# Performance work log

Measured on AMD Instinct MI355X. Metric: run time of the kernel, lower is better.

Reference implementation:

```python
import jax, jax.numpy as jnp
import numpy as np

FEATURE_DIM = 2048
NUM_HEADS = 16
NUM_KV_HEADS = 4
HEAD_DIM = 128
NEG = -1e9  # additive mask value for disallowed positions


def setup_inputs() -> dict:
    key = jax.random.key(0)
    ks = jax.random.split(key, 10)
    B, S = 1, 4096
    q_dim = NUM_HEADS * HEAD_DIM
    kv_dim = NUM_KV_HEADS * HEAD_DIM
    hidden_states = jax.random.normal(ks[0], (B, S, FEATURE_DIM), dtype=jnp.float32)
    # additive causal mask (B, 1, S, S): 0 on/below diagonal, large negative above
    causal = jnp.triu(jnp.full((S, S), NEG, dtype=jnp.float32), k=1)
    attention_mask = jnp.broadcast_to(causal, (B, 1, S, S))
    sd = 0.02
    Wq = jax.random.normal(ks[1], (q_dim, FEATURE_DIM), dtype=jnp.float32) * sd
    bq = jnp.zeros((q_dim,), dtype=jnp.float32)
    Wk = jax.random.normal(ks[2], (kv_dim, FEATURE_DIM), dtype=jnp.float32) * sd
    bk = jnp.zeros((kv_dim,), dtype=jnp.float32)
    Wv = jax.random.normal(ks[3], (kv_dim, FEATURE_DIM), dtype=jnp.float32) * sd
    bv = jnp.zeros((kv_dim,), dtype=jnp.float32)
    Wo = jax.random.normal(ks[4], (FEATURE_DIM, FEATURE_DIM), dtype=jnp.float32) * sd
    bo = jnp.zeros((FEATURE_DIM,), dtype=jnp.float32)
    return {
        "hidden_states": hidden_states,
        "attention_mask": attention_mask,
        "Wq": Wq, "bq": bq, "Wk": Wk, "bk": bk,
        "Wv": Wv, "bv": bv, "Wo": Wo, "bo": bo,
    }


def reference(hidden_states, attention_mask, Wq, bq, Wk, bk, Wv, bv, Wo, bo):
    B, S, _ = hidden_states.shape
    groups = NUM_HEADS // NUM_KV_HEADS
    scale = 1.0 / np.sqrt(HEAD_DIM)
    sigmoid_bias = jnp.asarray(-np.log(float(S)), dtype=hidden_states.dtype)

    # projections -> (B, H, S, D)
    q = (hidden_states @ Wq.T + bq).reshape(B, S, NUM_HEADS, HEAD_DIM).transpose(0, 2, 1, 3)
    k = (hidden_states @ Wk.T + bk).reshape(B, S, NUM_KV_HEADS, HEAD_DIM).transpose(0, 2, 1, 3)
    v = (hidden_states @ Wv.T + bv).reshape(B, S, NUM_KV_HEADS, HEAD_DIM).transpose(0, 2, 1, 3)

    # GQA: repeat kv heads to match query heads
    k = jnp.repeat(k, groups, axis=1)
    v = jnp.repeat(v, groups, axis=1)

    # sigmoid attention: QK^T * scale + mask + (-log S), sigmoid, then @V
    scores = jnp.einsum('bhqd,bhkd->bhqk', q, k) * scale
    scores = scores + attention_mask[:, :, :, :S]
    attn = jax.nn.sigmoid(scores + sigmoid_bias)
    out = jnp.einsum('bhqk,bhkd->bhqd', attn, v)

    out = out.transpose(0, 2, 1, 3).reshape(B, S, NUM_HEADS * HEAD_DIM)
    return out @ Wo.T + bo
```

## Files before the change

kernel.cpp:

```cpp
#include <hip/hip_runtime.h>

typedef __attribute__((ext_vector_type(8))) __bf16 bf16x8;
typedef __attribute__((ext_vector_type(4))) __bf16 bf16x4;
typedef __attribute__((ext_vector_type(4))) float  f32x4;

#define MFMA16(a, b, c) __builtin_amdgcn_mfma_f32_16x16x32_bf16((a), (b), (c), 0, 0, 0)

__device__ __forceinline__ void async16(const void* g, void* lds) {
    __builtin_amdgcn_global_load_lds(
        (__attribute__((address_space(1))) void*)(g),
        (__attribute__((address_space(3))) void*)(lds),
        16, 0, 0);
}

__global__ void cast_f32_bf16(const float* __restrict__ in, __bf16* __restrict__ out, int n) {
    int i = (blockIdx.x * blockDim.x + threadIdx.x) * 4;
    if (i >= n) return;
    f32x4 v = *(const f32x4*)(in + i);
    bf16x4 o;
    o[0] = (__bf16)v[0]; o[1] = (__bf16)v[1]; o[2] = (__bf16)v[2]; o[3] = (__bf16)v[3];
    *(bf16x4*)(out + i) = o;
}

#define BM 128
#define BN 128
#define BKK 32

template <typename OutT>
__global__ __launch_bounds__(256, 2) void gemm_bt(
    const __bf16* __restrict__ A,
    const __bf16* __restrict__ B0, OutT* __restrict__ C0, const float* __restrict__ b0, int N0,
    const __bf16* __restrict__ B1, OutT* __restrict__ C1, const float* __restrict__ b1, int N1,
    const __bf16* __restrict__ B2, OutT* __restrict__ C2, const float* __restrict__ b2, int N2,
    int K, bool transC2)
{
    const __bf16* Bm; OutT* Cm; const float* bias; int N;
    int z = blockIdx.z;
    if (z == 0)      { Bm = B0; Cm = C0; bias = b0; N = N0; }
    else if (z == 1) { Bm = B1; Cm = C1; bias = b1; N = N1; }
    else             { Bm = B2; Cm = C2; bias = b2; N = N2; }

    int n0 = blockIdx.x * BN;
    if (n0 >= N) return;
    int m0 = blockIdx.y * BM;

    __shared__ alignas(16) __bf16 As[BM * BKK];
    __shared__ alignas(16) __bf16 Bs[BN * BKK];

    int tid = threadIdx.x;
    int wv = tid >> 6, ln = tid & 63;
    int lr = ln >> 2, lc = ln & 3;
    int fr = ln & 15, fh = ln >> 4;

    int wr = wv >> 1, wc = wv & 1;

    f32x4 acc[4][4];
#pragma unroll
    for (int i = 0; i < 4; ++i)
#pragma unroll
        for (int j = 0; j < 4; ++j) acc[i][j] = (f32x4){0.f, 0.f, 0.f, 0.f};

    const __bf16* Ag = A  + (size_t)m0 * K;
    const __bf16* Bg = Bm + (size_t)n0 * K;

    for (int k0 = 0; k0 < K; k0 += BKK) {
#pragma unroll
        for (int half = 0; half < 2; ++half) {
            int row = wv * 32 + half * 16 + lr;
            async16(Ag + (size_t)row * K + k0 + lc * 8, &As[(wv * 32 + half * 16) * BKK]);
            async16(Bg + (size_t)row * K + k0 + lc * 8, &Bs[(wv * 32 + half * 16) * BKK]);
        }
        __syncthreads();

        bf16x8 af[4], bfr[4];
#pragma unroll
        for (int i = 0; i < 4; ++i) af[i]  = *(const bf16x8*)&As[(wr * 64 + i * 16 + fr) * BKK + fh * 8];
#pragma unroll
        for (int j = 0; j < 4; ++j) bfr[j] = *(const bf16x8*)&Bs[(wc * 64 + j * 16 + fr) * BKK + fh * 8];
#pragma unroll
        for (int i = 0; i < 4; ++i)
#pragma unroll
            for (int j = 0; j < 4; ++j)
                acc[i][j] = MFMA16(af[i], bfr[j], acc[i][j]);
        __syncthreads();
    }

    if constexpr (sizeof(OutT) == 2) {
        if (transC2 && z == 2) {
            const int M = (int)gridDim.y * BM;
            __bf16* Ct = (__bf16*)Cm;
#pragma unroll
            for (int j = 0; j < 4; ++j) {
                int col = n0 + wc * 64 + j * 16 + fr;
                float bv = bias[col];
#pragma unroll
                for (int i = 0; i < 4; ++i) {
                    int rbase = m0 + wr * 64 + i * 16 + fh * 4;
                    bf16x4 o;
#pragma unroll
                    for (int rq = 0; rq < 4; ++rq) o[rq] = (__bf16)(acc[i][j][rq] + bv);
                    *(bf16x4*)&Ct[(size_t)col * M + rbase] = o;
                }
            }
            return;
        }
    }

#pragma unroll
    for (int j = 0; j < 4; ++j) {
        int col = n0 + wc * 64 + j * 16 + fr;
        float bv = bias[col];
#pragma unroll
        for (int i = 0; i < 4; ++i) {
            int rbase = m0 + wr * 64 + i * 16 + fh * 4;
#pragma unroll
            for (int r = 0; r < 4; ++r) {
                float v = acc[i][j][r] + bv;
                Cm[(size_t)(rbase + r) * N + col] = (OutT)v;
            }
        }
    }
}

__global__ __launch_bounds__(256, 4) void attn_sigmoid(
    const __bf16* __restrict__ Qg, const __bf16* __restrict__ Kg,
    const __bf16* __restrict__ Vtg, __bf16* __restrict__ AO)
{
    const float SCALE = 0.08838834764831845f;
    const float SBIAS = -8.31776616671934f;

    int id = blockIdx.x;
    int rr = id >> 8, u = id & 255;
    int h = u & 15, g = u >> 4;
    int qt = (rr == 0) ? 63 - g : (rr == 1) ? 32 + g : (rr == 2) ? 31 - g : g;
    int kvh = h >> 2;

    int tid = threadIdx.x;
    int wv = tid >> 6, ln = tid & 63;
    int fr = ln & 15, fh = ln >> 4;

    __shared__ alignas(16) char KsB[16384];
    __shared__ alignas(16) char VtB[16384];
    __shared__ alignas(16) char PsB[8192];

    bf16x8 qf[4];
    {
        const __bf16* qp = Qg + (size_t)(qt * 64 + wv * 16 + fr) * 2048 + h * 128 + fh * 8;
#pragma unroll
        for (int dk = 0; dk < 4; ++dk) qf[dk] = *(const bf16x8*)(qp + dk * 32);
    }

    f32x4 oacc[8];
#pragma unroll
    for (int dn = 0; dn < 8; ++dn) oacc[dn] = (f32x4){0.f, 0.f, 0.f, 0.f};

    int nkt = qt + 1;
    for (int kt = 0; kt < nkt; ++kt) {
        {
            char* ksl = KsB + wv * 4096;
            char* vtl = VtB + wv * 4096;
#pragma unroll
            for (int i = 0; i < 4; ++i) {
                int r = wv * 16 + i * 4 + (ln >> 4);
                int c = (ln & 15) ^ (r & 15);
                async16(Kg + (size_t)(kt * 64 + r) * 512 + kvh * 128 + c * 8, ksl + i * 1024);
            }
#pragma unroll
            for (int i = 0; i < 4; ++i) {
                int d = wv * 32 + i * 8 + (ln >> 3);
                int c = (ln & 7) ^ (d & 7);
                async16(Vtg + (size_t)(kvh * 128 + d) * 4096 + kt * 64 + c * 8, vtl + i * 1024);
            }
        }
        __syncthreads();

        bool needmask = (kt == qt);
#pragma unroll
        for (int nj = 0; nj < 4; ++nj) {
            bf16x8 kf[4];
            int key = nj * 16 + fr;
#pragma unroll
            for (int dk = 0; dk < 4; ++dk)
                kf[dk] = *(const bf16x8*)(KsB + key * 256 + (((dk * 4 + fh) ^ (key & 15)) << 4));
            f32x4 sa = (f32x4){0.f, 0.f, 0.f, 0.f};
#pragma unroll
            for (int dk = 0; dk < 4; ++dk) sa = MFMA16(qf[dk], kf[dk], sa);
            int kr = nj * 16 + fr;
#pragma unroll
            for (int r = 0; r < 4; ++r) {
                int ql = wv * 16 + fh * 4 + r;
                float x = sa[r] * SCALE + SBIAS;
                float p = __fdividef(1.f, 1.f + __expf(-x));
                if (needmask && kr > ql) p = 0.f;
                *(__bf16*)(PsB + ql * 128 + (((kr >> 3) ^ (ql & 7)) << 4) + (kr & 7) * 2) = (__bf16)p;
            }
        }

        bf16x8 pf[2];
        {
            int q = wv * 16 + fr;
#pragma unroll
            for (int kk = 0; kk < 2; ++kk)
                pf[kk] = *(const bf16x8*)(PsB + q * 128 + (((kk * 4 + fh) ^ (q & 7)) << 4));
        }
#pragma unroll
        for (int dn = 0; dn < 8; ++dn) {
            int d = dn * 16 + fr;
            bf16x8 vf0 = *(const bf16x8*)(VtB + d * 128 + ((fh ^ (d & 7)) << 4));
            bf16x8 vf1 = *(const bf16x8*)(VtB + d * 128 + (((4 + fh) ^ (d & 7)) << 4));
            oacc[dn] = MFMA16(pf[0], vf0, oacc[dn]);
            oacc[dn] = MFMA16(pf[1], vf1, oacc[dn]);
        }
        __syncthreads();
    }

#pragma unroll
    for (int dn = 0; dn < 8; ++dn)
#pragma unroll
        for (int r = 0; r < 4; ++r)
            AO[(size_t)(qt * 64 + wv * 16 + fh * 4 + r) * 2048 + h * 128 + dn * 16 + fr]
                = (__bf16)oacc[dn][r];
}

extern "C" void kernel_launch(void* const* d_in, const int* in_sizes, int n_in,
                              void* d_out, int out_size, void* d_ws, size_t ws_size,
                              hipStream_t stream)
{
    const float* X  = (const float*)d_in[0];
    const float* Wq = (const float*)d_in[2];
    const float* bq = (const float*)d_in[3];
    const float* Wk = (const float*)d_in[4];
    const float* bk = (const float*)d_in[5];
    const float* Wv = (const float*)d_in[6];
    const float* bv = (const float*)d_in[7];
    const float* Wo = (const float*)d_in[8];
    const float* bo = (const float*)d_in[9];
    float* Out = (float*)d_out;

    if (ws_size < 54525952u) return;

    char* ws = (char*)d_ws;
    __bf16* Xb  = (__bf16*)(ws + 0);
    __bf16* Qb  = (__bf16*)(ws + 16777216);
    __bf16* Kb  = (__bf16*)(ws + 33554432);
    __bf16* Vb  = (__bf16*)(ws + 37748736);
    __bf16* Wqb = (__bf16*)(ws + 41943040);
    __bf16* Wkb = (__bf16*)(ws + 50331648);
    __bf16* Wvb = (__bf16*)(ws + 52428800);
    __bf16* AOb = Xb;
    __bf16* Wob = Wqb;

    cast_f32_bf16<<<8192, 256, 0, stream>>>(X,  Xb,  8388608);
    cast_f32_bf16<<<4096, 256, 0, stream>>>(Wq, Wqb, 4194304);
    cast_f32_bf16<<<1024, 256, 0, stream>>>(Wk, Wkb, 1048576);
    cast_f32_bf16<<<1024, 256, 0, stream>>>(Wv, Wvb, 1048576);

    gemm_bt<__bf16><<<dim3(16, 32, 3), 256, 0, stream>>>(Xb,
        Wqb, Qb, bq, 2048,
        Wkb, Kb, bk, 512,
        Wvb, Vb, bv, 512, 2048, true);

    cast_f32_bf16<<<4096, 256, 0, stream>>>(Wo, Wob, 4194304);

    attn_sigmoid<<<1024, 256, 0, stream>>>(Qb, Kb, Vb, AOb);

    gemm_bt<float><<<dim3(16, 32, 1), 256, 0, stream>>>(AOb,
        Wob, Out, bo, 2048,
        nullptr, nullptr, nullptr, 0,
        nullptr, nullptr, nullptr, 0, 2048, false);
}
```

Baseline: 461.0 us.

## Double query tile per attention block to reuse K/V tiles, use exp2/rcp sigmoid

Each attention block now handles 128 query rows (two 16-row sub-tiles per wave) instead of 64, so every K/V tile loaded into LDS feeds twice the MFMA work. The grid halves to 512 blocks, the causal scheduling order is simplified, and launch bounds drop to 3 blocks per SM to allow for the extra registers. The sigmoid is rewritten as a fused exp2 with folded scale and bias constants plus a hardware reciprocal. The trade-off is lower occupancy and coarser load balance across blocks of different causal length.

```diff
diff --git a/kernel.cpp b/kernel.cpp
--- a/kernel.cpp
+++ b/kernel.cpp
@@ -122,17 +122,17 @@
     }
 }
 
-__global__ __launch_bounds__(256, 4) void attn_sigmoid(
+__global__ __launch_bounds__(256, 3) void attn_sigmoid(
     const __bf16* __restrict__ Qg, const __bf16* __restrict__ Kg,
     const __bf16* __restrict__ Vtg, __bf16* __restrict__ AO)
 {
-    const float SCALE = 0.08838834764831845f;
-    const float SBIAS = -8.31776616671934f;
+    const float C1 = -0.12752551286084110f;
+    const float C2 = 12.0f;
 
     int id = blockIdx.x;
     int rr = id >> 8, u = id & 255;
     int h = u & 15, g = u >> 4;
-    int qt = (rr == 0) ? 63 - g : (rr == 1) ? 32 + g : (rr == 2) ? 31 - g : g;
+    int qt = rr ? g : 31 - g;
     int kvh = h >> 2;
 
     int tid = threadIdx.x;
@@ -141,20 +141,23 @@
 
     __shared__ alignas(16) char KsB[16384];
     __shared__ alignas(16) char VtB[16384];
-    __shared__ alignas(16) char PsB[8192];
-
-    bf16x8 qf[4];
-    {
-        const __bf16* qp = Qg + (size_t)(qt * 64 + wv * 16 + fr) * 2048 + h * 128 + fh * 8;
-#pragma unroll
-        for (int dk = 0; dk < 4; ++dk) qf[dk] = *(const bf16x8*)(qp + dk * 32);
-    }
-
-    f32x4 oacc[8];
-#pragma unroll
-    for (int dn = 0; dn < 8; ++dn) oacc[dn] = (f32x4){0.f, 0.f, 0.f, 0.f};
-
-    int nkt = qt + 1;
+    __shared__ alignas(16) char PsB[16384];
+
+    bf16x8 qf[2][4];
+#pragma unroll
+    for (int mi = 0; mi < 2; ++mi) {
+        const __bf16* qp = Qg + (size_t)(qt * 128 + wv * 32 + mi * 16 + fr) * 2048 + h * 128 + fh * 8;
+#pragma unroll
+        for (int dk = 0; dk < 4; ++dk) qf[mi][dk] = *(const bf16x8*)(qp + dk * 32);
+    }
+
+    f32x4 oacc[2][8];
+#pragma unroll
+    for (int mi = 0; mi < 2; ++mi)
+#pragma unroll
+        for (int dn = 0; dn < 8; ++dn) oacc[mi][dn] = (f32x4){0.f, 0.f, 0.f, 0.f};
+
+    int nkt = 2 * qt + 2;
     for (int kt = 0; kt < nkt; ++kt) {
         {
             char* ksl = KsB + wv * 4096;
@@ -174,7 +177,7 @@
         }
         __syncthreads();
 
-        bool needmask = (kt == qt);
+        bool needmask = (kt >= 2 * qt);
 #pragma unroll
         for (int nj = 0; nj < 4; ++nj) {
             bf16x8 kf[4];
@@ -182,44 +185,55 @@
 #pragma unroll
             for (int dk = 0; dk < 4; ++dk)
                 kf[dk] = *(const bf16x8*)(KsB + key * 256 + (((dk * 4 + fh) ^ (key & 15)) << 4));
-            f32x4 sa = (f32x4){0.f, 0.f, 0.f, 0.f};
-#pragma unroll
-            for (int dk = 0; dk < 4; ++dk) sa = MFMA16(qf[dk], kf[dk], sa);
             int kr = nj * 16 + fr;
-#pragma unroll
-            for (int r = 0; r < 4; ++r) {
-                int ql = wv * 16 + fh * 4 + r;
-                float x = sa[r] * SCALE + SBIAS;
-                float p = __fdividef(1.f, 1.f + __expf(-x));
-                if (needmask && kr > ql) p = 0.f;
-                *(__bf16*)(PsB + ql * 128 + (((kr >> 3) ^ (ql & 7)) << 4) + (kr & 7) * 2) = (__bf16)p;
-            }
-        }
-
-        bf16x8 pf[2];
-        {
-            int q = wv * 16 + fr;
+            int keyg = kt * 64 + kr;
+#pragma unroll
+            for (int mi = 0; mi < 2; ++mi) {
+                f32x4 sa = (f32x4){0.f, 0.f, 0.f, 0.f};
+#pragma unroll
+                for (int dk = 0; dk < 4; ++dk) sa = MFMA16(qf[mi][dk], kf[dk], sa);
+                int qb = wv * 32 + mi * 16 + fh * 4;
+#pragma unroll
+                for (int r = 0; r < 4; ++r) {
+                    int ql = qb + r;
+                    float e = __builtin_amdgcn_exp2f(fmaf(sa[r], C1, C2));
+                    float p = __builtin_amdgcn_rcpf(1.f + e);
+                    if (needmask && keyg > qt * 128 + ql) p = 0.f;
+                    *(__bf16*)(PsB + ql * 128 + (((kr >> 3) ^ (ql & 7)) << 4) + (kr & 7) * 2) = (__bf16)p;
+                }
+            }
+        }
+
+        bf16x8 pf[2][2];
+#pragma unroll
+        for (int mi = 0; mi < 2; ++mi) {
+            int q = wv * 32 + mi * 16 + fr;
 #pragma unroll
             for (int kk = 0; kk < 2; ++kk)
-                pf[kk] = *(const bf16x8*)(PsB + q * 128 + (((kk * 4 + fh) ^ (q & 7)) << 4));
+                pf[mi][kk] = *(const bf16x8*)(PsB + q * 128 + (((kk * 4 + fh) ^ (q & 7)) << 4));
         }
 #pragma unroll
         for (int dn = 0; dn < 8; ++dn) {
             int d = dn * 16 + fr;
             bf16x8 vf0 = *(const bf16x8*)(VtB + d * 128 + ((fh ^ (d & 7)) << 4));
             bf16x8 vf1 = *(const bf16x8*)(VtB + d * 128 + (((4 + fh) ^ (d & 7)) << 4));
-            oacc[dn] = MFMA16(pf[0], vf0, oacc[dn]);
-            oacc[dn] = MFMA16(pf[1], vf1, oacc[dn]);
-        }
-        __syncthreads();
-    }
-
-#pragma unroll
-    for (int dn = 0; dn < 8; ++dn)
-#pragma unroll
-        for (int r = 0; r < 4; ++r)
-            AO[(size_t)(qt * 64 + wv * 16 + fh * 4 + r) * 2048 + h * 128 + dn * 16 + fr]
-                = (__bf16)oacc[dn][r];
+#pragma unroll
+            for (int mi = 0; mi < 2; ++mi) {
+                oacc[mi][dn] = MFMA16(pf[mi][0], vf0, oacc[mi][dn]);
+                oacc[mi][dn] = MFMA16(pf[mi][1], vf1, oacc[mi][dn]);
+            }
+        }
+        __syncthreads();
+    }
+
+#pragma unroll
+    for (int mi = 0; mi < 2; ++mi)
+#pragma unroll
+        for (int dn = 0; dn < 8; ++dn)
+#pragma unroll
+            for (int r = 0; r < 4; ++r)
+                AO[(size_t)(qt * 128 + wv * 32 + mi * 16 + fh * 4 + r) * 2048 + h * 128 + dn * 16 + fr]
+                    = (__bf16)oacc[mi][dn][r];
 }
 
 extern "C" void kernel_launch(void* const* d_in, const int* in_sizes, int n_in,
@@ -262,7 +276,7 @@
 
     cast_f32_bf16<<<4096, 256, 0, stream>>>(Wo, Wob, 4194304);
 
-    attn_sigmoid<<<1024, 256, 0, stream>>>(Qb, Kb, Vb, AOb);
+    attn_sigmoid<<<512, 256, 0, stream>>>(Qb, Kb, Vb, AOb);
 
     gemm_bt<float><<<dim3(16, 32, 1), 256, 0, stream>>>(AOb,
         Wob, Out, bo, 2048,
```

New measurement: 549.7 us. 1.19x slower.
